# Optimization experiments

Hardware: AMD Instinct MI355X
Metric: run time of the kernel (lower is better)

Reference implementation:

```python
import jax, jax.numpy as jnp
import numpy as np
import math

D_MODEL = 512
HEADS = 8
GRID_COUNT = 40000
MAX_LEN = 5000


def _positional_embedding(d_model, max_len=MAX_LEN):
    pe = np.zeros((max_len, d_model), dtype=np.float32)
    position = np.arange(max_len, dtype=np.float32)[:, None]
    div_term = np.exp(np.arange(0, d_model, 2, dtype=np.float32) * -(math.log(10000.0) / d_model))
    pe[:, 0::2] = np.sin(position * div_term)
    pe[:, 1::2] = np.cos(position * div_term)
    return jnp.asarray(pe)  # [max_len, d_model]


def _mha(q, k, v, wq, bq, wk, bk, wv, bv, heads):
    # Faithful to SelfAttention: no 1/sqrt(d_k) scaling in the original.
    B, Sq, D = q.shape
    Sk = k.shape[1]
    dh = D // heads
    Q = (q @ wq.T + bq).reshape(B, Sq, heads, dh)
    K = (k @ wk.T + bk).reshape(B, Sk, heads, dh)
    V = (v @ wv.T + bv).reshape(B, Sk, heads, dh)
    attn = jax.nn.softmax(jnp.einsum('bqhd,bkhd->bhqk', Q, K), axis=-1)
    out = jnp.einsum('bhqk,bkhd->bqhd', attn, V)
    return out.reshape(B, Sq, D)


def setup_inputs() -> dict:
    key = jax.random.key(0)
    ks = jax.random.split(key, 20)
    B, S_CURR, S_HIST, N_MASK = 32, 128, 256, 16
    s = 1.0 / math.sqrt(D_MODEL)

    def lin(k):
        kw, kb = jax.random.split(k)
        w = jax.random.uniform(kw, (D_MODEL, D_MODEL), jnp.float32, -s, s)
        b = jax.random.uniform(kb, (D_MODEL,), jnp.float32, -s, s)
        return w, b

    h_wq, h_bq = lin(ks[0]); h_wk, h_bk = lin(ks[1]); h_wv, h_bv = lin(ks[2])
    c_wq, c_bq = lin(ks[3]); c_wk, c_bk = lin(ks[4]); c_wv, c_bv = lin(ks[5])
    x_wq, x_bq = lin(ks[6]); x_wk, x_bk = lin(ks[7]); x_wv, x_bv = lin(ks[8])
    t2_w, t2_b = lin(ks[9])
    emb = jax.random.normal(ks[10], (GRID_COUNT, D_MODEL), jnp.float32)

    return {
        'hist_traj_grid': jax.random.randint(ks[11], (B, S_HIST), 0, GRID_COUNT),
        'userId': jax.random.randint(ks[12], (B,), 0, 1000),
        'mask_pos': jax.random.randint(ks[13], (B, N_MASK), 0, S_CURR),
        'mask_curr_traj_grid': jax.random.randint(ks[14], (B, S_CURR), 0, GRID_COUNT),
        'aggregator_hist_traj_grid': jax.random.randint(ks[15], (B, S_HIST), 0, GRID_COUNT),
        'emb': emb,
        'h_wq': h_wq, 'h_bq': h_bq, 'h_wk': h_wk, 'h_bk': h_bk, 'h_wv': h_wv, 'h_bv': h_bv,
        'c_wq': c_wq, 'c_bq': c_bq, 'c_wk': c_wk, 'c_bk': c_bk, 'c_wv': c_wv, 'c_bv': c_bv,
        'x_wq': x_wq, 'x_bq': x_bq, 'x_wk': x_wk, 'x_bk': x_bk, 'x_wv': x_wv, 'x_bv': x_bv,
        't2_w': t2_w, 't2_b': t2_b,
    }


def reference(hist_traj_grid, userId, mask_pos, mask_curr_traj_grid, aggregator_hist_traj_grid,
              emb,
              h_wq, h_bq, h_wk, h_bk, h_wv, h_bv,
              c_wq, c_bq, c_wk, c_bk, c_wv, c_bv,
              x_wq, x_bq, x_wk, x_bk, x_wv, x_bv,
              t2_w, t2_b):
    pe = _positional_embedding(D_MODEL)
    hist = emb[aggregator_hist_traj_grid]          # [B, S_hist, D]
    curr = emb[mask_curr_traj_grid]                # [B, S_curr, D]
    hist = hist + pe[None, :hist.shape[1]]
    curr = curr + pe[None, :curr.shape[1]]

    hist = _mha(hist, hist, hist, h_wq, h_bq, h_wk, h_bk, h_wv, h_bv, HEADS)
    curr = _mha(curr, curr, curr, c_wq, c_bq, c_wk, c_bk, c_wv, c_bv, HEADS)
    _cross = _mha(curr, hist, hist, x_wq, x_bq, x_wk, x_bk, x_wv, x_bv, HEADS)
    # NOTE: original overwrites liner_transform output with liner_transform2(tanh(curr)),
    # so cross-attention output and liner_transform do not affect the result.
    hyb = jnp.tanh(curr) @ t2_w.T + t2_b           # [B, S_curr, D]

    # index_select of flattened [B*S, D] at mask_pos + b*S == take_along_axis over seq dim
    gathered = jnp.take_along_axis(hyb, mask_pos[:, :, None], axis=1)  # [B, n_mask, D]
    gathered = gathered.reshape(-1, D_MODEL)

    candidate = emb[2:]                            # [vocab-2, D]
    scores = gathered @ candidate.T                # [B*n_mask, vocab-2]
    return jax.nn.log_softmax(scores, axis=-1)
```

## Files before the change

### kernel.cpp

```cpp
#include <hip/hip_runtime.h>
#include <hip/hip_bf16.h>
#include <math.h>
#include <float.h>

#define B       32
#define S_CURR  128
#define D       512
#define H       8
#define DH      64
#define NM      16
#define NCAND   39998
#define MG      (B * NM)
#define SCLD    40064
#define NT      313

typedef __bf16 bf16x8_t __attribute__((ext_vector_type(8)));
typedef float  f32x4_t  __attribute__((ext_vector_type(4)));

typedef __attribute__((address_space(3))) unsigned int lds_u32_t;
typedef const __attribute__((address_space(1))) unsigned int gbl_u32_t;

__device__ __forceinline__ void async16(const void* g, void* l) {
    __builtin_amdgcn_global_load_lds((gbl_u32_t*)g, (lds_u32_t*)l, 16, 0, 0);
}

__global__ __launch_bounds__(256) void convert_all(
    const float* __restrict__ emb,
    const float* __restrict__ wq, const float* __restrict__ wk,
    const float* __restrict__ wv, const float* __restrict__ t2w,
    __bf16* __restrict__ embB, __bf16* __restrict__ wqB, __bf16* __restrict__ wkB,
    __bf16* __restrict__ wvB, __bf16* __restrict__ t2wB)
{
    int bx = blockIdx.x;
    const float* src; __bf16* dst; size_t n, base;
    if (bx < 10000) {
        src = emb + 2 * D; dst = embB; n = (size_t)NCAND * D; base = (size_t)bx * 2048;
    } else {
        int w = (bx - 10000) >> 7;
        base = (size_t)((bx - 10000) & 127) * 2048;
        n = (size_t)D * D;
        src = (w == 0) ? wq : (w == 1) ? wk : (w == 2) ? wv : t2w;
        dst = (w == 0) ? wqB : (w == 1) ? wkB : (w == 2) ? wvB : t2wB;
    }
    size_t i = base + (size_t)threadIdx.x * 8;
    if (i >= n) return;
    float4 a = *(const float4*)(src + i);
    float4 b = *(const float4*)(src + i + 4);
    bf16x8_t v;
    v[0] = (__bf16)a.x; v[1] = (__bf16)a.y; v[2] = (__bf16)a.z; v[3] = (__bf16)a.w;
    v[4] = (__bf16)b.x; v[5] = (__bf16)b.y; v[6] = (__bf16)b.z; v[7] = (__bf16)b.w;
    *(bf16x8_t*)(dst + i) = v;
}

__global__ __launch_bounds__(256) void build_curr(const int* __restrict__ idx,
                                                  const float* __restrict__ emb,
                                                  __bf16* __restrict__ currB,
                                                  const int* __restrict__ mask_pos,
                                                  int* __restrict__ qidx) {
    int bs = blockIdx.x;
    if (bs == B * S_CURR) {
        int r = threadIdx.x;
        qidx[r] = (r >> 4) * S_CURR + mask_pos[r];
        r += 256;
        qidx[r] = (r >> 4) * S_CURR + mask_pos[r];
        return;
    }
    int s = bs & (S_CURR - 1);
    int g = idx[bs];
    const float* e = emb + (size_t)g * D;
    __bf16* o = currB + (size_t)bs * D;
    int d = threadIdx.x * 2;
    float div = expf(-(float)d * (9.210340371976184f / 512.0f));
    float ang = (float)s * div;
    o[d]     = (__bf16)(e[d]     + sinf(ang));
    o[d + 1] = (__bf16)(e[d + 1] + cosf(ang));
}

__global__ __launch_bounds__(256) void gemm_bf(
    const __bf16* __restrict__ A,
    const __bf16* __restrict__ W0, const float* __restrict__ b0, __bf16* __restrict__ C0,
    const __bf16* __restrict__ W1, const float* __restrict__ b1, __bf16* __restrict__ C1,
    const int* __restrict__ rowidx)
{
    const __bf16* W = blockIdx.z ? W1 : W0;
    const float* bias = blockIdx.z ? b1 : b0;
    __bf16* C = blockIdx.z ? C1 : C0;

    __shared__ __bf16 As[128 * 64];
    __shared__ __bf16 Bs[128 * 64];

    const int tid = threadIdx.x, lane = tid & 63, wave = tid >> 6;
    const int wy = wave >> 1, wx = wave & 1;
    const int m0 = blockIdx.x * 128, n0 = blockIdx.y * 128;
    const int lrow = lane >> 3, lcol = (lane & 7) * 8;

    const __bf16* aptr[4]; const __bf16* bptr[4];
#pragma unroll
    for (int i = 0; i < 4; ++i) {
        int chunk = wave * 4 + i;
        int ar = m0 + chunk * 8 + lrow;
        if (rowidx) ar = rowidx[ar];
        aptr[i] = A + (size_t)ar * 512 + lcol;
        bptr[i] = W + (size_t)(n0 + chunk * 8 + lrow) * 512 + lcol;
    }

    f32x4_t acc[4][4];
#pragma unroll
    for (int i = 0; i < 4; ++i)
#pragma unroll
        for (int j = 0; j < 4; ++j) acc[i][j] = (f32x4_t){0.f, 0.f, 0.f, 0.f};

    for (int kk = 0; kk < 512; kk += 64) {
#pragma unroll
        for (int i = 0; i < 4; ++i) {
            int chunk = wave * 4 + i;
            async16(aptr[i] + kk, &As[chunk * 512]);
            async16(bptr[i] + kk, &Bs[chunk * 512]);
        }
        __syncthreads();
#pragma unroll
        for (int kb = 0; kb < 2; ++kb) {
            const int ko = kb * 32 + (lane >> 4) * 8;
            bf16x8_t af[4], bfv[4];
#pragma unroll
            for (int i = 0; i < 4; ++i)
                af[i] = *(const bf16x8_t*)&As[(wy * 64 + i * 16 + (lane & 15)) * 64 + ko];
#pragma unroll
            for (int j = 0; j < 4; ++j)
                bfv[j] = *(const bf16x8_t*)&Bs[(wx * 64 + j * 16 + (lane & 15)) * 64 + ko];
#pragma unroll
            for (int i = 0; i < 4; ++i)
#pragma unroll
                for (int j = 0; j < 4; ++j)
                    acc[i][j] = __builtin_amdgcn_mfma_f32_16x16x32_bf16(
                        af[i], bfv[j], acc[i][j], 0, 0, 0);
        }
        __syncthreads();
    }

    const int colq = lane & 15, quad = lane >> 4;
#pragma unroll
    for (int i = 0; i < 4; ++i)
#pragma unroll
        for (int j = 0; j < 4; ++j) {
            int col = n0 + wx * 64 + j * 16 + colq;
            float bv = bias[col];
#pragma unroll
            for (int rr = 0; rr < 4; ++rr) {
                int row = m0 + wy * 64 + i * 16 + quad * 4 + rr;
                C[(size_t)row * 512 + col] = (__bf16)(acc[i][j][rr] + bv);
            }
        }
}

__global__ __launch_bounds__(256) void gemm_scores(
    const __bf16* __restrict__ A,
    const __bf16* __restrict__ Bm,
    __bf16* __restrict__ scB,
    float* __restrict__ pmax, float* __restrict__ psum)
{
    __shared__ __bf16 As[128 * 64];
    __shared__ __bf16 Bs[128 * 64];
    __shared__ float redm[2][128], reds[2][128];

    const int tid = threadIdx.x, lane = tid & 63, wave = tid >> 6;
    const int wy = wave >> 1, wx = wave & 1;
    const int m0 = blockIdx.x * 128, n0 = blockIdx.y * 128;
    const int lrow = lane >> 3, lcol = (lane & 7) * 8;

    const __bf16* aptr[4]; const __bf16* bptr[4];
#pragma unroll
    for (int i = 0; i < 4; ++i) {
        int chunk = wave * 4 + i;
        aptr[i] = A + (size_t)(m0 + chunk * 8 + lrow) * 512 + lcol;
        bptr[i] = Bm + (size_t)(n0 + chunk * 8 + lrow) * 512 + lcol;
    }

    f32x4_t acc[4][4];
#pragma unroll
    for (int i = 0; i < 4; ++i)
#pragma unroll
        for (int j = 0; j < 4; ++j) acc[i][j] = (f32x4_t){0.f, 0.f, 0.f, 0.f};

    for (int kk = 0; kk < 512; kk += 64) {
#pragma unroll
        for (int i = 0; i < 4; ++i) {
            int chunk = wave * 4 + i;
            async16(aptr[i] + kk, &As[chunk * 512]);
            async16(bptr[i] + kk, &Bs[chunk * 512]);
        }
        __syncthreads();
#pragma unroll
        for (int kb = 0; kb < 2; ++kb) {
            const int ko = kb * 32 + (lane >> 4) * 8;
            bf16x8_t af[4], bfv[4];
#pragma unroll
            for (int i = 0; i < 4; ++i)
                af[i] = *(const bf16x8_t*)&As[(wy * 64 + i * 16 + (lane & 15)) * 64 + ko];
#pragma unroll
            for (int j = 0; j < 4; ++j)
                bfv[j] = *(const bf16x8_t*)&Bs[(wx * 64 + j * 16 + (lane & 15)) * 64 + ko];
#pragma unroll
            for (int i = 0; i < 4; ++i)
#pragma unroll
                for (int j = 0; j < 4; ++j)
                    acc[i][j] = __builtin_amdgcn_mfma_f32_16x16x32_bf16(
                        af[i], bfv[j], acc[i][j], 0, 0, 0);
        }
        __syncthreads();
    }

    const int colq = lane & 15, quad = lane >> 4;
#pragma unroll
    for (int i = 0; i < 4; ++i) {
#pragma unroll
        for (int rr = 0; rr < 4; ++rr) {
            const int row = wy * 64 + i * 16 + quad * 4 + rr;
            const size_t rowbase = (size_t)(m0 + row) * SCLD;
            float v[4]; float m = -FLT_MAX;
#pragma unroll
            for (int j = 0; j < 4; ++j) {
                int col = n0 + wx * 64 + j * 16 + colq;
                __bf16 xb = (__bf16)acc[i][j][rr];
                if (col < NCAND) {
                    scB[rowbase + col] = xb;
                    float xr = (float)xb;
                    v[j] = xr; m = fmaxf(m, xr);
                } else v[j] = -FLT_MAX;
            }
            float s = 0.f;
#pragma unroll
            for (int j = 0; j < 4; ++j)
                s += (v[j] > -FLT_MAX) ? __expf(v[j] - m) : 0.f;
#pragma unroll
            for (int mk = 1; mk < 16; mk <<= 1) {
                float om = __shfl_xor(m, mk);
                float os = __shfl_xor(s, mk);
                float mm = fmaxf(m, om);
                s = s * __expf(m - mm) + os * __expf(om - mm);
                m = mm;
            }
            if (colq == 0) { redm[wx][row] = m; reds[wx][row] = s; }
        }
    }
    __syncthreads();
    if (tid < 128) {
        float ma = redm[0][tid], sa = reds[0][tid];
        float mb = redm[1][tid], sb = reds[1][tid];
        float mm = fmaxf(ma, mb);
        float ss = sa * __expf(ma - mm) + sb * __expf(mb - mm);
        pmax[(size_t)blockIdx.y * MG + m0 + tid] = mm;
        psum[(size_t)blockIdx.y * MG + m0 + tid] = ss;
    }
}

__global__ __launch_bounds__(128) void attn_kernel(const __bf16* __restrict__ Q,
                                                   const __bf16* __restrict__ K,
                                                   const __bf16* __restrict__ V,
                                                   __bf16* __restrict__ attnB) {
    int r = blockIdx.x, h = blockIdx.y, b = r >> 4, t = threadIdx.x;

    __shared__ float qv[DH];
    __shared__ float p[S_CURR];
    __shared__ float red[S_CURR];

    if (t < DH) qv[t] = (float)Q[(size_t)r * D + h * DH + t];
    __syncthreads();

    const __bf16* Krow = K + ((size_t)(b * S_CURR + t)) * D + h * DH;
    float s = 0.f;
#pragma unroll
    for (int d = 0; d < DH; d += 8) {
        bf16x8_t kv = *(const bf16x8_t*)(Krow + d);
#pragma unroll
        for (int q = 0; q < 8; ++q) s += qv[d + q] * (float)kv[q];
    }
    red[t] = s;
    __syncthreads();
    for (int off = 64; off > 0; off >>= 1) {
        if (t < off) red[t] = fmaxf(red[t], red[t + off]);
        __syncthreads();
    }
    float m = red[0];
    __syncthreads();
    float e = __expf(s - m);
    p[t] = e; red[t] = e;
    __syncthreads();
    for (int off = 64; off > 0; off >>= 1) {
        if (t < off) red[t] += red[t + off];
        __syncthreads();
    }
    float inv = 1.0f / red[0];
    __syncthreads();

    int d = t & 63, half = t >> 6;
    float acc = 0.f;
    for (int k2 = half * 64; k2 < half * 64 + 64; ++k2)
        acc += p[k2] * (float)V[((size_t)(b * S_CURR + k2)) * D + h * DH + d];
    red[t] = acc;
    __syncthreads();
    if (t < 64)
        attnB[(size_t)r * D + h * DH + d] = (__bf16)tanhf((red[t] + red[t + 64]) * inv);
}

__global__ __launch_bounds__(256) void lse_reduce(const float* __restrict__ pmax,
                                                  const float* __restrict__ psum,
                                                  float* __restrict__ lse) {
    int row = blockIdx.x, t = threadIdx.x;
    float m = -FLT_MAX, s = 0.f;
    for (int i = t; i < NT; i += 256) {
        float om = pmax[(size_t)i * MG + row];
        float os = psum[(size_t)i * MG + row];
        float mm = fmaxf(m, om);
        s = s * __expf(m - mm) + os * __expf(om - mm);
        m = mm;
    }
    __shared__ float ms[256], ss[256];
    ms[t] = m; ss[t] = s;
    __syncthreads();
    for (int off = 128; off > 0; off >>= 1) {
        if (t < off) {
            float m1 = ms[t], s1 = ss[t], m2 = ms[t + off], s2 = ss[t + off];
            float mm = fmaxf(m1, m2);
            ms[t] = mm;
            ss[t] = s1 * __expf(m1 - mm) + s2 * __expf(m2 - mm);
        }
        __syncthreads();
    }
    if (t == 0) lse[row] = ms[0] + logf(ss[0]);
}

__global__ __launch_bounds__(256) void final_out(const __bf16* __restrict__ scB,
                                                 const float* __restrict__ lse,
                                                 float* __restrict__ out) {
    int row = blockIdx.y;
    int c0 = (blockIdx.x * 256 + threadIdx.x) * 8;
    if (c0 >= NCAND) return;
    float l = lse[row];
    bf16x8_t v = *(const bf16x8_t*)(scB + (size_t)row * SCLD + c0);
    float* o = out + (size_t)row * NCAND + c0;
    if (c0 + 8 <= NCAND) {
        *(float2*)(o)     = make_float2((float)v[0] - l, (float)v[1] - l);
        *(float2*)(o + 2) = make_float2((float)v[2] - l, (float)v[3] - l);
        *(float2*)(o + 4) = make_float2((float)v[4] - l, (float)v[5] - l);
        *(float2*)(o + 6) = make_float2((float)v[6] - l, (float)v[7] - l);
    } else {
        for (int k2 = 0; k2 < NCAND - c0; ++k2) o[k2] = (float)v[k2] - l;
    }
}

extern "C" void kernel_launch(void* const* d_in, const int* in_sizes, int n_in,
                              void* d_out, int out_size, void* d_ws, size_t ws_size,
                              hipStream_t stream) {
    const int*   mask_pos = (const int*)d_in[2];
    const int*   curr_idx = (const int*)d_in[3];
    const float* emb      = (const float*)d_in[5];
    const float* c_bq = (const float*)d_in[13];
    const float* c_wq = (const float*)d_in[12];
    const float* c_wk = (const float*)d_in[14];
    const float* c_bk = (const float*)d_in[15];
    const float* c_wv = (const float*)d_in[16];
    const float* c_bv = (const float*)d_in[17];
    const float* t2_w = (const float*)d_in[24];
    const float* t2_b = (const float*)d_in[25];
    float* out = (float*)d_out;

    char* w = (char*)d_ws;
    __bf16* embB  = (__bf16*)w;
    __bf16* scB   = (__bf16*)(w + 41025536);
    __bf16* currB = scB;
    __bf16* Kf    = (__bf16*)(w + 41025536 + 4194304);
    __bf16* Vf    = (__bf16*)(w + 41025536 + 8388608);
    __bf16* Qg    = (__bf16*)(w + 41025536 + 12582912);
    __bf16* attnB = (__bf16*)(w + 41025536 + 13107200);
    __bf16* wqB   = (__bf16*)(w + 41025536 + 13631488);
    __bf16* wkB   = (__bf16*)(w + 41025536 + 14155776);
    __bf16* wvB   = (__bf16*)(w + 41025536 + 14680064);
    __bf16* t2wB  = (__bf16*)(w + 41025536 + 15204352);
    int*    qidx  = (int*)   (w + 41025536 + 15728640);
    __bf16* gatheredB = (__bf16*)(w + 82051072);
    float*  pmax  = (float*)(w + 82575360);
    float*  psum  = (float*)(w + 83216384);
    float*  lse   = (float*)(w + 83857408);

    hipLaunchKernelGGL(convert_all, dim3(10512), dim3(256), 0, stream,
                       emb, c_wq, c_wk, c_wv, t2_w, embB, wqB, wkB, wvB, t2wB);
    hipLaunchKernelGGL(build_curr, dim3(B * S_CURR + 1), dim3(256), 0, stream,
                       curr_idx, emb, currB, mask_pos, qidx);
    hipLaunchKernelGGL(gemm_bf, dim3(4, 4, 1), dim3(256), 0, stream,
                       currB, wqB, c_bq, Qg, wqB, c_bq, Qg, qidx);
    hipLaunchKernelGGL(gemm_bf, dim3(32, 4, 2), dim3(256), 0, stream,
                       currB, wkB, c_bk, Kf, wvB, c_bv, Vf, (const int*)nullptr);
    hipLaunchKernelGGL(attn_kernel, dim3(MG, H), dim3(128), 0, stream,
                       Qg, Kf, Vf, attnB);
    hipLaunchKernelGGL(gemm_bf, dim3(4, 4, 1), dim3(256), 0, stream,
                       attnB, t2wB, t2_b, gatheredB, t2wB, t2_b, gatheredB,
                       (const int*)nullptr);
    hipLaunchKernelGGL(gemm_scores, dim3(4, NT), dim3(256), 0, stream,
                       gatheredB, embB, scB, pmax, psum);
    hipLaunchKernelGGL(lse_reduce, dim3(MG), dim3(256), 0, stream, pmax, psum, lse);
    hipLaunchKernelGGL(final_out, dim3(20, MG), dim3(256), 0, stream, scB, lse, out);
}
```

Baseline: 341.8 us.

## Fuse prep kernels, merge QKV GEMMs, swizzle LDS, XCD-aware scores grid, batched attention

Merges the conversion and curr-building kernels into one launch, and folds the Q projection into the K/V GEMM launch as a third z-slice. Adds an XOR swizzle on the LDS tile layout in both GEMMs to reduce bank conflicts, and remaps the scores GEMM grid so that tiles sharing the same candidate block are placed on the same XCD. Rewrites attention so one block handles all 16 queries of a batch/head, staging K and V once in LDS. These aim to cut launch overhead, LDS conflicts and redundant K/V reads, at the cost of more complex indexing.

Result: faster. 305.6 us (-10.6%).

```diff
diff --git a/kernel.cpp b/kernel.cpp
--- a/kernel.cpp
+++ b/kernel.cpp
@@ -24,49 +24,47 @@
     __builtin_amdgcn_global_load_lds((gbl_u32_t*)g, (lds_u32_t*)l, 16, 0, 0);
 }
 
-__global__ __launch_bounds__(256) void convert_all(
+__global__ __launch_bounds__(256) void prep_kernel(
     const float* __restrict__ emb,
     const float* __restrict__ wq, const float* __restrict__ wk,
     const float* __restrict__ wv, const float* __restrict__ t2w,
     __bf16* __restrict__ embB, __bf16* __restrict__ wqB, __bf16* __restrict__ wkB,
-    __bf16* __restrict__ wvB, __bf16* __restrict__ t2wB)
+    __bf16* __restrict__ wvB, __bf16* __restrict__ t2wB,
+    const int* __restrict__ curr_idx, __bf16* __restrict__ currB,
+    const int* __restrict__ mask_pos, int* __restrict__ qidx)
 {
     int bx = blockIdx.x;
-    const float* src; __bf16* dst; size_t n, base;
-    if (bx < 10000) {
-        src = emb + 2 * D; dst = embB; n = (size_t)NCAND * D; base = (size_t)bx * 2048;
-    } else {
-        int w = (bx - 10000) >> 7;
-        base = (size_t)((bx - 10000) & 127) * 2048;
-        n = (size_t)D * D;
-        src = (w == 0) ? wq : (w == 1) ? wk : (w == 2) ? wv : t2w;
-        dst = (w == 0) ? wqB : (w == 1) ? wkB : (w == 2) ? wvB : t2wB;
-    }
-    size_t i = base + (size_t)threadIdx.x * 8;
-    if (i >= n) return;
-    float4 a = *(const float4*)(src + i);
-    float4 b = *(const float4*)(src + i + 4);
-    bf16x8_t v;
-    v[0] = (__bf16)a.x; v[1] = (__bf16)a.y; v[2] = (__bf16)a.z; v[3] = (__bf16)a.w;
-    v[4] = (__bf16)b.x; v[5] = (__bf16)b.y; v[6] = (__bf16)b.z; v[7] = (__bf16)b.w;
-    *(bf16x8_t*)(dst + i) = v;
-}
-
-__global__ __launch_bounds__(256) void build_curr(const int* __restrict__ idx,
-                                                  const float* __restrict__ emb,
-                                                  __bf16* __restrict__ currB,
-                                                  const int* __restrict__ mask_pos,
-                                                  int* __restrict__ qidx) {
-    int bs = blockIdx.x;
-    if (bs == B * S_CURR) {
+    if (bx < 10512) {
+        const float* src; __bf16* dst; size_t n, base;
+        if (bx < 10000) {
+            src = emb + 2 * D; dst = embB; n = (size_t)NCAND * D; base = (size_t)bx * 2048;
+        } else {
+            int w = (bx - 10000) >> 7;
+            base = (size_t)((bx - 10000) & 127) * 2048;
+            n = (size_t)D * D;
+            src = (w == 0) ? wq : (w == 1) ? wk : (w == 2) ? wv : t2w;
+            dst = (w == 0) ? wqB : (w == 1) ? wkB : (w == 2) ? wvB : t2wB;
+        }
+        size_t i = base + (size_t)threadIdx.x * 8;
+        if (i >= n) return;
+        float4 a = *(const float4*)(src + i);
+        float4 b = *(const float4*)(src + i + 4);
+        bf16x8_t v;
+        v[0] = (__bf16)a.x; v[1] = (__bf16)a.y; v[2] = (__bf16)a.z; v[3] = (__bf16)a.w;
+        v[4] = (__bf16)b.x; v[5] = (__bf16)b.y; v[6] = (__bf16)b.z; v[7] = (__bf16)b.w;
+        *(bf16x8_t*)(dst + i) = v;
+        return;
+    }
+    if (bx == 14608) {
         int r = threadIdx.x;
         qidx[r] = (r >> 4) * S_CURR + mask_pos[r];
         r += 256;
         qidx[r] = (r >> 4) * S_CURR + mask_pos[r];
         return;
     }
+    int bs = bx - 10512;
     int s = bs & (S_CURR - 1);
-    int g = idx[bs];
+    int g = curr_idx[bs];
     const float* e = emb + (size_t)g * D;
     __bf16* o = currB + (size_t)bs * D;
     int d = threadIdx.x * 2;
@@ -80,11 +78,14 @@
     const __bf16* __restrict__ A,
     const __bf16* __restrict__ W0, const float* __restrict__ b0, __bf16* __restrict__ C0,
     const __bf16* __restrict__ W1, const float* __restrict__ b1, __bf16* __restrict__ C1,
+    const __bf16* __restrict__ W2, const float* __restrict__ b2, __bf16* __restrict__ C2,
     const int* __restrict__ rowidx)
 {
-    const __bf16* W = blockIdx.z ? W1 : W0;
-    const float* bias = blockIdx.z ? b1 : b0;
-    __bf16* C = blockIdx.z ? C1 : C0;
+    const int z = blockIdx.z;
+    if (z == 2 && blockIdx.x >= 4) return;
+    const __bf16* W = (z == 0) ? W0 : (z == 1) ? W1 : W2;
+    const float* bias = (z == 0) ? b0 : (z == 1) ? b1 : b2;
+    __bf16* C = (z == 0) ? C0 : (z == 1) ? C1 : C2;
 
     __shared__ __bf16 As[128 * 64];
     __shared__ __bf16 Bs[128 * 64];
@@ -92,14 +93,15 @@
     const int tid = threadIdx.x, lane = tid & 63, wave = tid >> 6;
     const int wy = wave >> 1, wx = wave & 1;
     const int m0 = blockIdx.x * 128, n0 = blockIdx.y * 128;
-    const int lrow = lane >> 3, lcol = (lane & 7) * 8;
+    const int lrow = lane >> 3;
+    const int lcol = (((lane & 7) ^ lrow) & 7) * 8;
 
     const __bf16* aptr[4]; const __bf16* bptr[4];
 #pragma unroll
     for (int i = 0; i < 4; ++i) {
         int chunk = wave * 4 + i;
         int ar = m0 + chunk * 8 + lrow;
-        if (rowidx) ar = rowidx[ar];
+        if (z == 2) ar = rowidx[ar];
         aptr[i] = A + (size_t)ar * 512 + lcol;
         bptr[i] = W + (size_t)(n0 + chunk * 8 + lrow) * 512 + lcol;
     }
@@ -109,6 +111,8 @@
     for (int i = 0; i < 4; ++i)
 #pragma unroll
         for (int j = 0; j < 4; ++j) acc[i][j] = (f32x4_t){0.f, 0.f, 0.f, 0.f};
+
+    const int l7 = lane & 7, quad = lane >> 4, c16 = lane & 15;
 
     for (int kk = 0; kk < 512; kk += 64) {
 #pragma unroll
@@ -120,14 +124,14 @@
         __syncthreads();
 #pragma unroll
         for (int kb = 0; kb < 2; ++kb) {
-            const int ko = kb * 32 + (lane >> 4) * 8;
+            const int goff = (((kb * 4 + quad) ^ l7)) * 8;
             bf16x8_t af[4], bfv[4];
 #pragma unroll
             for (int i = 0; i < 4; ++i)
-                af[i] = *(const bf16x8_t*)&As[(wy * 64 + i * 16 + (lane & 15)) * 64 + ko];
+                af[i] = *(const bf16x8_t*)&As[(wy * 64 + i * 16 + c16) * 64 + goff];
 #pragma unroll
             for (int j = 0; j < 4; ++j)
-                bfv[j] = *(const bf16x8_t*)&Bs[(wx * 64 + j * 16 + (lane & 15)) * 64 + ko];
+                bfv[j] = *(const bf16x8_t*)&Bs[(wx * 64 + j * 16 + c16) * 64 + goff];
 #pragma unroll
             for (int i = 0; i < 4; ++i)
 #pragma unroll
@@ -138,12 +142,11 @@
         __syncthreads();
     }
 
-    const int colq = lane & 15, quad = lane >> 4;
 #pragma unroll
     for (int i = 0; i < 4; ++i)
 #pragma unroll
         for (int j = 0; j < 4; ++j) {
-            int col = n0 + wx * 64 + j * 16 + colq;
+            int col = n0 + wx * 64 + j * 16 + c16;
             float bv = bias[col];
 #pragma unroll
             for (int rr = 0; rr < 4; ++rr) {
@@ -159,14 +162,20 @@
     __bf16* __restrict__ scB,
     float* __restrict__ pmax, float* __restrict__ psum)
 {
+    const int bid = blockIdx.x;
+    const int xcd = bid & 7, k = bid >> 3;
+    const int nt = xcd * 40 + (k >> 2);
+    if (nt >= NT) return;
+    const int m0 = (k & 3) * 128, n0 = nt * 128;
+
     __shared__ __bf16 As[128 * 64];
     __shared__ __bf16 Bs[128 * 64];
     __shared__ float redm[2][128], reds[2][128];
 
     const int tid = threadIdx.x, lane = tid & 63, wave = tid >> 6;
     const int wy = wave >> 1, wx = wave & 1;
-    const int m0 = blockIdx.x * 128, n0 = blockIdx.y * 128;
-    const int lrow = lane >> 3, lcol = (lane & 7) * 8;
+    const int lrow = lane >> 3;
+    const int lcol = (((lane & 7) ^ lrow) & 7) * 8;
 
     const __bf16* aptr[4]; const __bf16* bptr[4];
 #pragma unroll
@@ -182,6 +191,8 @@
 #pragma unroll
         for (int j = 0; j < 4; ++j) acc[i][j] = (f32x4_t){0.f, 0.f, 0.f, 0.f};
 
+    const int l7 = lane & 7, quad = lane >> 4, c16 = lane & 15;
+
     for (int kk = 0; kk < 512; kk += 64) {
 #pragma unroll
         for (int i = 0; i < 4; ++i) {
@@ -192,14 +203,14 @@
         __syncthreads();
 #pragma unroll
         for (int kb = 0; kb < 2; ++kb) {
-            const int ko = kb * 32 + (lane >> 4) * 8;
+            const int goff = (((kb * 4 + quad) ^ l7)) * 8;
             bf16x8_t af[4], bfv[4];
 #pragma unroll
             for (int i = 0; i < 4; ++i)
-                af[i] = *(const bf16x8_t*)&As[(wy * 64 + i * 16 + (lane & 15)) * 64 + ko];
+                af[i] = *(const bf16x8_t*)&As[(wy * 64 + i * 16 + c16) * 64 + goff];
 #pragma unroll
             for (int j = 0; j < 4; ++j)
-                bfv[j] = *(const bf16x8_t*)&Bs[(wx * 64 + j * 16 + (lane & 15)) * 64 + ko];
+                bfv[j] = *(const bf16x8_t*)&Bs[(wx * 64 + j * 16 + c16) * 64 + goff];
 #pragma unroll
             for (int i = 0; i < 4; ++i)
 #pragma unroll
@@ -210,7 +221,6 @@
         __syncthreads();
     }
 
-    const int colq = lane & 15, quad = lane >> 4;
 #pragma unroll
     for (int i = 0; i < 4; ++i) {
 #pragma unroll
@@ -220,7 +230,7 @@
             float v[4]; float m = -FLT_MAX;
 #pragma unroll
             for (int j = 0; j < 4; ++j) {
-                int col = n0 + wx * 64 + j * 16 + colq;
+                int col = n0 + wx * 64 + j * 16 + c16;
                 __bf16 xb = (__bf16)acc[i][j][rr];
                 if (col < NCAND) {
                     scB[rowbase + col] = xb;
@@ -240,7 +250,7 @@
                 s = s * __expf(m - mm) + os * __expf(om - mm);
                 m = mm;
             }
-            if (colq == 0) { redm[wx][row] = m; reds[wx][row] = s; }
+            if (c16 == 0) { redm[wx][row] = m; reds[wx][row] = s; }
         }
     }
     __syncthreads();
@@ -249,58 +259,75 @@
         float mb = redm[1][tid], sb = reds[1][tid];
         float mm = fmaxf(ma, mb);
         float ss = sa * __expf(ma - mm) + sb * __expf(mb - mm);
-        pmax[(size_t)blockIdx.y * MG + m0 + tid] = mm;
-        psum[(size_t)blockIdx.y * MG + m0 + tid] = ss;
-    }
-}
-
-__global__ __launch_bounds__(128) void attn_kernel(const __bf16* __restrict__ Q,
+        pmax[(size_t)nt * MG + m0 + tid] = mm;
+        psum[(size_t)nt * MG + m0 + tid] = ss;
+    }
+}
+
+#define KPAD 72
+__global__ __launch_bounds__(256) void attn_kernel(const __bf16* __restrict__ Qg,
                                                    const __bf16* __restrict__ K,
                                                    const __bf16* __restrict__ V,
                                                    __bf16* __restrict__ attnB) {
-    int r = blockIdx.x, h = blockIdx.y, b = r >> 4, t = threadIdx.x;
-
-    __shared__ float qv[DH];
-    __shared__ float p[S_CURR];
-    __shared__ float red[S_CURR];
-
-    if (t < DH) qv[t] = (float)Q[(size_t)r * D + h * DH + t];
+    const int b = blockIdx.x, h = blockIdx.y, t = threadIdx.x;
+    __shared__ __bf16 Ks[128 * KPAD];
+    __shared__ __bf16 Vs[128 * KPAD];
+    __shared__ float  Qs[16 * 68];
+    __shared__ float  P[16 * 130];
+
+    for (int i = t; i < 1024; i += 256) {
+        int row = i >> 3, cg = (i & 7) * 8;
+        size_t gsrc = ((size_t)(b * S_CURR + row)) * D + h * DH + cg;
+        *(bf16x8_t*)&Ks[row * KPAD + cg] = *(const bf16x8_t*)&K[gsrc];
+        *(bf16x8_t*)&Vs[row * KPAD + cg] = *(const bf16x8_t*)&V[gsrc];
+    }
+    if (t < 128) {
+        int q = t >> 3, cg = (t & 7) * 8;
+        bf16x8_t qv = *(const bf16x8_t*)&Qg[((size_t)(b * NM + q)) * D + h * DH + cg];
+#pragma unroll
+        for (int u = 0; u < 8; ++u) Qs[q * 68 + cg + u] = (float)qv[u];
+    }
     __syncthreads();
 
-    const __bf16* Krow = K + ((size_t)(b * S_CURR + t)) * D + h * DH;
-    float s = 0.f;
-#pragma unroll
-    for (int d = 0; d < DH; d += 8) {
-        bf16x8_t kv = *(const bf16x8_t*)(Krow + d);
-#pragma unroll
-        for (int q = 0; q < 8; ++q) s += qv[d + q] * (float)kv[q];
-    }
-    red[t] = s;
-    __syncthreads();
-    for (int off = 64; off > 0; off >>= 1) {
-        if (t < off) red[t] = fmaxf(red[t], red[t + off]);
-        __syncthreads();
-    }
-    float m = red[0];
-    __syncthreads();
-    float e = __expf(s - m);
-    p[t] = e; red[t] = e;
-    __syncthreads();
-    for (int off = 64; off > 0; off >>= 1) {
-        if (t < off) red[t] += red[t + off];
-        __syncthreads();
-    }
-    float inv = 1.0f / red[0];
-    __syncthreads();
-
-    int d = t & 63, half = t >> 6;
-    float acc = 0.f;
-    for (int k2 = half * 64; k2 < half * 64 + 64; ++k2)
-        acc += p[k2] * (float)V[((size_t)(b * S_CURR + k2)) * D + h * DH + d];
-    red[t] = acc;
-    __syncthreads();
-    if (t < 64)
-        attnB[(size_t)r * D + h * DH + d] = (__bf16)tanhf((red[t] + red[t + 64]) * inv);
+    const int q = t >> 4, i = t & 15;
+    float sv[8];
+    float lmax = -FLT_MAX;
+#pragma unroll
+    for (int z = 0; z < 8; ++z) {
+        int kk = i + z * 16;
+        float s = 0.f;
+#pragma unroll
+        for (int d0 = 0; d0 < DH; d0 += 8) {
+            bf16x8_t kv = *(const bf16x8_t*)&Ks[kk * KPAD + d0];
+#pragma unroll
+            for (int u = 0; u < 8; ++u) s += Qs[q * 68 + d0 + u] * (float)kv[u];
+        }
+        sv[z] = s; lmax = fmaxf(lmax, s);
+    }
+#pragma unroll
+    for (int mk = 1; mk < 16; mk <<= 1) lmax = fmaxf(lmax, __shfl_xor(lmax, mk));
+    float lsum = 0.f;
+#pragma unroll
+    for (int z = 0; z < 8; ++z) {
+        float e = __expf(sv[z] - lmax);
+        P[q * 130 + i + z * 16] = e;
+        lsum += e;
+    }
+#pragma unroll
+    for (int mk = 1; mk < 16; mk <<= 1) lsum += __shfl_xor(lsum, mk);
+    const float inv = 1.0f / lsum;
+
+    const int d = i * 4;
+    float a0 = 0.f, a1 = 0.f, a2 = 0.f, a3 = 0.f;
+    for (int kk = 0; kk < 128; ++kk) {
+        float p = P[q * 130 + kk];
+        const __bf16* vr = &Vs[kk * KPAD + d];
+        a0 += p * (float)vr[0]; a1 += p * (float)vr[1];
+        a2 += p * (float)vr[2]; a3 += p * (float)vr[3];
+    }
+    __bf16* o = attnB + ((size_t)(b * NM + q)) * D + h * DH + d;
+    o[0] = (__bf16)tanhf(a0 * inv); o[1] = (__bf16)tanhf(a1 * inv);
+    o[2] = (__bf16)tanhf(a2 * inv); o[3] = (__bf16)tanhf(a3 * inv);
 }
 
 __global__ __launch_bounds__(256) void lse_reduce(const float* __restrict__ pmax,
@@ -355,8 +382,8 @@
     const int*   mask_pos = (const int*)d_in[2];
     const int*   curr_idx = (const int*)d_in[3];
     const float* emb      = (const float*)d_in[5];
+    const float* c_wq = (const float*)d_in[12];
     const float* c_bq = (const float*)d_in[13];
-    const float* c_wq = (const float*)d_in[12];
     const float* c_wk = (const float*)d_in[14];
     const float* c_bk = (const float*)d_in[15];
     const float* c_wv = (const float*)d_in[16];
@@ -383,20 +410,18 @@
     float*  psum  = (float*)(w + 83216384);
     float*  lse   = (float*)(w + 83857408);
 
-    hipLaunchKernelGGL(convert_all, dim3(10512), dim3(256), 0, stream,
-                       emb, c_wq, c_wk, c_wv, t2_w, embB, wqB, wkB, wvB, t2wB);
-    hipLaunchKernelGGL(build_curr, dim3(B * S_CURR + 1), dim3(256), 0, stream,
-                       curr_idx, emb, currB, mask_pos, qidx);
-    hipLaunchKernelGGL(gemm_bf, dim3(4, 4, 1), dim3(256), 0, stream,
-                       currB, wqB, c_bq, Qg, wqB, c_bq, Qg, qidx);
-    hipLaunchKernelGGL(gemm_bf, dim3(32, 4, 2), dim3(256), 0, stream,
-                       currB, wkB, c_bk, Kf, wvB, c_bv, Vf, (const int*)nullptr);
-    hipLaunchKernelGGL(attn_kernel, dim3(MG, H), dim3(128), 0, stream,
+    hipLaunchKernelGGL(prep_kernel, dim3(14609), dim3(256), 0, stream,
+                       emb, c_wq, c_wk, c_wv, t2_w, embB, wqB, wkB, wvB, t2wB,
+                       curr_idx, currB, mask_pos, qidx);
+    hipLaunchKernelGGL(gemm_bf, dim3(32, 4, 3), dim3(256), 0, stream,
+                       currB, wkB, c_bk, Kf, wvB, c_bv, Vf, wqB, c_bq, Qg, qidx);
+    hipLaunchKernelGGL(attn_kernel, dim3(B, H), dim3(256), 0, stream,
                        Qg, Kf, Vf, attnB);
     hipLaunchKernelGGL(gemm_bf, dim3(4, 4, 1), dim3(256), 0, stream,
-                       attnB, t2wB, t2_b, gatheredB, t2wB, t2_b, gatheredB,
+                       attnB, t2wB, t2_b, gatheredB,
+                       t2wB, t2_b, gatheredB, t2wB, t2_b, gatheredB,
                        (const int*)nullptr);
-    hipLaunchKernelGGL(gemm_scores, dim3(4, NT), dim3(256), 0, stream,
+    hipLaunchKernelGGL(gemm_scores, dim3(1280), dim3(256), 0, stream,
                        gatheredB, embB, scB, pmax, psum);
     hipLaunchKernelGGL(lse_reduce, dim3(MG), dim3(256), 0, stream, pmax, psum, lse);
     hipLaunchKernelGGL(final_out, dim3(20, MG), dim3(256), 0, stream, scB, lse, out);
```
